# Kernel optimization log

Measured on AMD Instinct MI355X. Metric: run time of the kernel, lower is better.

Reference implementation:

```python
import jax, jax.numpy as jnp
import numpy as np

N_FEATURES = 64
D_MODEL = 256


def setup_inputs() -> dict:
    key = jax.random.key(0)
    ks = jax.random.split(key, 6)
    B = 4096
    x = jax.random.normal(ks[0], (B, N_FEATURES), dtype=jnp.float32)
    # Stacked per-feature weights (equivalent to n_features separate MLPs).
    # Linear(1, d): weight [d, 1] -> stacked as [F, d]; bias [F, d]
    s1 = 1.0  # kaiming-uniform-ish scale for fan_in=1
    W1 = jax.random.uniform(ks[1], (N_FEATURES, D_MODEL), jnp.float32, -s1, s1)
    b1 = jax.random.uniform(ks[2], (N_FEATURES, D_MODEL), jnp.float32, -s1, s1)
    # Linear(d, d): weight [d, d] per feature -> [F, d, d]
    s2 = 1.0 / np.sqrt(D_MODEL)
    W2 = jax.random.uniform(ks[3], (N_FEATURES, D_MODEL, D_MODEL), jnp.float32, -s2, s2)
    b2 = jax.random.uniform(ks[4], (N_FEATURES, D_MODEL), jnp.float32, -s2, s2)
    cls_token = jax.random.normal(ks[5], (1, 1, D_MODEL), dtype=jnp.float32)
    return {"x": x, "W1": W1, "b1": b1, "W2": W2, "b2": b2, "cls_token": cls_token}


def reference(x, W1, b1, W2, b2, cls_token):
    # h[b,f,d] = relu(x[b,f] * W1[f,d] + b1[f,d])   (Linear(1,d) per feature)
    h = jax.nn.relu(x[:, :, None] * W1[None, :, :] + b1[None, :, :])
    # out[b,f,e] = h[b,f,:] @ W2[f,:,:] + b2[f,:]   (Linear(d,d) per feature)
    out = jnp.einsum("bfd,fde->bfe", h, W2) + b2[None, :, :]
    cls = jnp.broadcast_to(cls_token, (x.shape[0], 1, out.shape[-1]))
    return jnp.concatenate([cls, out], axis=1)  # [B, F+1, d_model]
```

## Files before the change

kernel.cpp:

```cpp
#include <hip/hip_runtime.h>
#include <hip/hip_bf16.h>


#define B_  4096
#define F_  64
#define D_  256
#define ORS (65 * 256)

using f32x4  = __attribute__((ext_vector_type(4))) float;
using s16x8  = __attribute__((ext_vector_type(8))) short;

__device__ __forceinline__ unsigned short to_bf16_bits(float v) {
    __hip_bfloat16 h = __float2bfloat16(v);
    return *reinterpret_cast<unsigned short*>(&h);
}

__global__ __launch_bounds__(256) void femb_prep(
    const float* __restrict__ W2, unsigned short* __restrict__ W2r)
{
    const int blk = blockIdx.x;
    const int f   = blk >> 2;
    const int kq  = blk & 3;
    const int t   = threadIdx.x;

    const float* col = W2 + (size_t)f * D_ * D_ + (size_t)(kq * 64) * D_ + t;
    float r[64];
    #pragma unroll
    for (int j = 0; j < 64; ++j) r[j] = col[(size_t)j * D_];

    const int w   = t >> 6;
    const int nt  = (t >> 4) & 3;
    const int llo = t & 15;

    #pragma unroll
    for (int j8 = 0; j8 < 8; ++j8) {
        union { s16x8 s; unsigned short u[8]; } pk;
        #pragma unroll
        for (int e = 0; e < 8; ++e) pk.u[e] = to_bf16_bits(r[j8 * 8 + e]);
        const int ks   = kq * 2 + (j8 >> 2);
        const int lhi  = j8 & 3;
        const size_t unit = ((size_t)((f * 4 + w) * 4 + nt) * 8 + ks) * 64 + lhi * 16 + llo;
        *reinterpret_cast<s16x8*>(W2r + unit * 8) = pk.s;
    }
}

__global__ __launch_bounds__(256, 2) void femb_main10(
    const float* __restrict__ x,  const float* __restrict__ W1,
    const float* __restrict__ b1, const unsigned short* __restrict__ W2r,
    const float* __restrict__ b2, const float* __restrict__ cls,
    float* __restrict__ out)
{
    __shared__ float w1s[D_];
    __shared__ float b1s[D_];
    __shared__ float xs[512];
    __shared__ __align__(16) float eb[2][16 * 260];

    const int tid  = threadIdx.x;
    const int bid  = blockIdx.x;
    const int f    = bid & 63;
    const int row0 = (bid >> 6) << 9;

    w1s[tid] = W1[f * D_ + tid];
    b1s[tid] = b1[f * D_ + tid];
    xs[tid]       = x[(size_t)(row0 + tid) * F_ + f];
    xs[256 + tid] = x[(size_t)(row0 + 256 + tid) * F_ + f];

    const int lane = tid & 63;
    const int w    = tid >> 6;
    const int llo  = lane & 15;
    const int lhi  = lane >> 4;

    s16x8 breg[4][8];
    const unsigned short* gb = W2r + (size_t)(f * 4 + w) * 16384;
    #pragma unroll
    for (int nt = 0; nt < 4; ++nt)
        #pragma unroll
        for (int ks = 0; ks < 8; ++ks)
            breg[nt][ks] = *reinterpret_cast<const s16x8*>(
                gb + ((nt * 8 + ks) * 64 + lane) * 8);

    __syncthreads();

    f32x4 b2v  = *reinterpret_cast<const f32x4*>(&b2[f * D_ + lane * 4]);
    f32x4 clsv = *reinterpret_cast<const f32x4*>(cls + lane * 4);

#define EPI_BAR()                                                              \
    do {                                                                       \
        asm volatile("s_waitcnt lgkmcnt(0)" ::: "memory");                     \
        __builtin_amdgcn_s_barrier();                                          \
        asm volatile("" ::: "memory");                                         \
    } while (0)

    for (int ch = 0; ch < 16; ++ch) {
        const float xv0 = xs[ch * 32 + llo];
        const float xv1 = xs[ch * 32 + 16 + llo];

        f32x4 acc[2][4];
        #pragma unroll
        for (int mt = 0; mt < 2; ++mt)
            #pragma unroll
            for (int nt = 0; nt < 4; ++nt)
                acc[mt][nt] = (f32x4){0.f, 0.f, 0.f, 0.f};

        #pragma unroll
        for (int ks = 0; ks < 8; ++ks) {
            const int kg = ks * 32 + lhi * 8;
            f32x4 w1a = *reinterpret_cast<const f32x4*>(&w1s[kg]);
            f32x4 w1b = *reinterpret_cast<const f32x4*>(&w1s[kg + 4]);
            f32x4 b1a = *reinterpret_cast<const f32x4*>(&b1s[kg]);
            f32x4 b1b = *reinterpret_cast<const f32x4*>(&b1s[kg + 4]);

            s16x8 afrag[2];
            #pragma unroll
            for (int mt = 0; mt < 2; ++mt) {
                const float xv = mt ? xv1 : xv0;
                union { s16x8 sv; unsigned short u[8]; } pk;
                #pragma unroll
                for (int e = 0; e < 4; ++e) {
                    pk.u[e]     = to_bf16_bits(fmaxf(fmaf(xv, w1a[e], b1a[e]), 0.f));
                    pk.u[e + 4] = to_bf16_bits(fmaxf(fmaf(xv, w1b[e], b1b[e]), 0.f));
                }
                afrag[mt] = pk.sv;
            }

            #pragma unroll
            for (int nt = 0; nt < 4; ++nt)
                #pragma unroll
                for (int mt = 0; mt < 2; ++mt)
                    acc[mt][nt] = __builtin_amdgcn_mfma_f32_16x16x32_bf16(
                        breg[nt][ks], afrag[mt], acc[mt][nt], 0, 0, 0);
        }

        #pragma unroll
        for (int sc = 0; sc < 2; ++sc) {
            float* ebuf = eb[sc];
            #pragma unroll
            for (int nt = 0; nt < 4; ++nt)
                *reinterpret_cast<f32x4*>(
                    &ebuf[llo * 260 + w * 64 + nt * 16 + lhi * 4]) = acc[sc][nt];
            EPI_BAR();
            #pragma unroll
            for (int i = 0; i < 4; ++i) {
                const int lr = w * 4 + i;
                const size_t grow = (size_t)(row0 + ch * 32 + sc * 16 + lr);
                f32x4 v = *reinterpret_cast<const f32x4*>(&ebuf[lr * 260 + lane * 4]) + b2v;
                *reinterpret_cast<f32x4*>(out + grow * ORS + (f + 1) * D_ + lane * 4) = v;
                if (f == 0)
                    *reinterpret_cast<f32x4*>(out + grow * ORS + lane * 4) = clsv;
            }
            if (sc == 1) EPI_BAR();
        }
    }
#undef EPI_BAR
}

__global__ void femb_cls(const float* __restrict__ cls, float* __restrict__ out)
{
    int i = blockIdx.x * 256 + threadIdx.x;
    int b = i >> 6;
    int q = i & 63;
    f32x4 v = *reinterpret_cast<const f32x4*>(cls + q * 4);
    *reinterpret_cast<f32x4*>(out + (size_t)b * ORS + q * 4) = v;
}

__global__ __launch_bounds__(256, 2) void femb_main_fb(
    const float* __restrict__ x,  const float* __restrict__ W1,
    const float* __restrict__ b1, const float* __restrict__ W2,
    const float* __restrict__ b2, float* __restrict__ out)
{
    __shared__ float w1s[D_];
    __shared__ float b1s[D_];
    __shared__ float xs[128];
    __shared__ __align__(16) unsigned short bW[256][72];

    const int tid  = threadIdx.x;
    const int bid  = blockIdx.x;
    const int f    = bid & 63;
    const int row0 = (bid >> 6) << 7;

    w1s[tid] = W1[f * D_ + tid];
    b1s[tid] = b1[f * D_ + tid];
    if (tid < 128) xs[tid] = x[(size_t)(row0 + tid) * F_ + f];

    const int lane = tid & 63;
    const int wid  = tid >> 6;
    const int wm   = wid >> 1;
    const int wn   = wid & 1;
    const int llo  = lane & 15;
    const int lhi  = lane >> 4;

    __syncthreads();

    float xv[4];
    #pragma unroll
    for (int mt = 0; mt < 4; ++mt) xv[mt] = xs[wm * 64 + mt * 16 + llo];

    f32x4 acc[4][8];
    #pragma unroll
    for (int mt = 0; mt < 4; ++mt)
        #pragma unroll
        for (int nt = 0; nt < 8; ++nt)
            acc[mt][nt] = (f32x4){0.f, 0.f, 0.f, 0.f};

    const float* w2col = W2 + (size_t)f * D_ * D_ + tid;

    for (int kb = 0; kb < 4; ++kb) {
        float r[64];
        const float* p = w2col + (size_t)(kb * 64) * D_;
        #pragma unroll
        for (int j = 0; j < 64; ++j) r[j] = p[(size_t)j * D_];

        __syncthreads();
        #pragma unroll
        for (int j8 = 0; j8 < 8; ++j8) {
            union { s16x8 s; unsigned short u[8]; } pk;
            #pragma unroll
            for (int e = 0; e < 8; ++e) pk.u[e] = to_bf16_bits(r[j8 * 8 + e]);
            *reinterpret_cast<s16x8*>(&bW[tid][j8 * 8]) = pk.s;
        }
        __syncthreads();

        #pragma unroll
        for (int ks = 0; ks < 2; ++ks) {
            const int kg = kb * 64 + ks * 32 + lhi * 8;
            float w1r[8], b1r[8];
            #pragma unroll
            for (int e = 0; e < 8; ++e) { w1r[e] = w1s[kg + e]; b1r[e] = b1s[kg + e]; }

            s16x8 afrag[4];
            #pragma unroll
            for (int mt = 0; mt < 4; ++mt) {
                union { s16x8 s; unsigned short u[8]; } pk;
                #pragma unroll
                for (int e = 0; e < 8; ++e) {
                    float h = fmaf(xv[mt], w1r[e], b1r[e]);
                    pk.u[e] = to_bf16_bits(fmaxf(h, 0.f));
                }
                afrag[mt] = pk.s;
            }

            const int kl = ks * 32 + lhi * 8;
            #pragma unroll
            for (int nt = 0; nt < 8; ++nt) {
                s16x8 bfrag = *reinterpret_cast<const s16x8*>(
                    &bW[wn * 128 + nt * 16 + llo][kl]);
                #pragma unroll
                for (int mt = 0; mt < 4; ++mt)
                    acc[mt][nt] = __builtin_amdgcn_mfma_f32_16x16x32_bf16(
                        bfrag, afrag[mt], acc[mt][nt], 0, 0, 0);
            }
        }
    }

    const float* b2f = b2 + f * D_;
    float* obase = out + (size_t)(row0 + wm * 64 + llo) * ORS
                       + (f + 1) * D_ + wn * 128 + lhi * 4;
    #pragma unroll
    for (int nt = 0; nt < 8; ++nt) {
        f32x4 bv = *reinterpret_cast<const f32x4*>(&b2f[wn * 128 + nt * 16 + lhi * 4]);
        #pragma unroll
        for (int mt = 0; mt < 4; ++mt) {
            f32x4 v = acc[mt][nt] + bv;
            *reinterpret_cast<f32x4*>(obase + (size_t)mt * 16 * ORS + nt * 16) = v;
        }
    }
}

extern "C" void kernel_launch(void* const* d_in, const int* in_sizes, int n_in,
                              void* d_out, int out_size, void* d_ws, size_t ws_size,
                              hipStream_t stream)
{
    const float* x   = (const float*)d_in[0];
    const float* W1  = (const float*)d_in[1];
    const float* b1  = (const float*)d_in[2];
    const float* W2  = (const float*)d_in[3];
    const float* b2  = (const float*)d_in[4];
    const float* cls = (const float*)d_in[5];
    float* out = (float*)d_out;

    const size_t need = (size_t)F_ * D_ * D_ * sizeof(unsigned short);
    if (ws_size >= need) {
        unsigned short* W2r = (unsigned short*)d_ws;
        femb_prep<<<F_ * 4, 256, 0, stream>>>(W2, W2r);
        femb_main10<<<F_ * (B_ / 512), 256, 0, stream>>>(x, W1, b1, W2r, b2, cls, out);
    } else {
        femb_cls<<<(B_ * 64) / 256, 256, 0, stream>>>(cls, out);
        femb_main_fb<<<F_ * (B_ / 128), 256, 0, stream>>>(x, W1, b1, W2, b2, out);
    }
}
```

Baseline: 68.81 us.

## Process two features per 512-thread block for contiguous 2KB output row writes

Each block now handles two adjacent features over 256 batch rows with 8 waves, so every output row segment written is 512 contiguous floats (two features) instead of 256. The b2 bias is folded into the accumulator before the LDS staging store, and the grid doubles in rows while halving per-block chunk count. This aims to improve write coalescing and store efficiency on the output-bandwidth-bound epilogue, at the cost of larger LDS usage and an extra barrier per subchunk.

```diff
diff --git a/kernel.cpp b/kernel.cpp
--- a/kernel.cpp
+++ b/kernel.cpp
@@ -28,7 +28,7 @@
     #pragma unroll
     for (int j = 0; j < 64; ++j) r[j] = col[(size_t)j * D_];
 
-    const int w   = t >> 6;
+    const int cg  = t >> 6;
     const int nt  = (t >> 4) & 3;
     const int llo = t & 15;
 
@@ -39,39 +39,46 @@
         for (int e = 0; e < 8; ++e) pk.u[e] = to_bf16_bits(r[j8 * 8 + e]);
         const int ks   = kq * 2 + (j8 >> 2);
         const int lhi  = j8 & 3;
-        const size_t unit = ((size_t)((f * 4 + w) * 4 + nt) * 8 + ks) * 64 + lhi * 16 + llo;
+        const size_t unit = ((size_t)((f * 4 + cg) * 4 + nt) * 8 + ks) * 64 + lhi * 16 + llo;
         *reinterpret_cast<s16x8*>(W2r + unit * 8) = pk.s;
     }
 }
 
-__global__ __launch_bounds__(256, 2) void femb_main10(
+__global__ __launch_bounds__(512, 2) void femb_main11(
     const float* __restrict__ x,  const float* __restrict__ W1,
     const float* __restrict__ b1, const unsigned short* __restrict__ W2r,
     const float* __restrict__ b2, const float* __restrict__ cls,
     float* __restrict__ out)
 {
-    __shared__ float w1s[D_];
-    __shared__ float b1s[D_];
-    __shared__ float xs[512];
-    __shared__ __align__(16) float eb[2][16 * 260];
+    __shared__ float w1s[2][D_];
+    __shared__ float b1s[2][D_];
+    __shared__ float xs[2][256];
+    __shared__ __align__(16) float eb[2][16 * 516];
 
     const int tid  = threadIdx.x;
     const int bid  = blockIdx.x;
-    const int f    = bid & 63;
-    const int row0 = (bid >> 6) << 9;
-
-    w1s[tid] = W1[f * D_ + tid];
-    b1s[tid] = b1[f * D_ + tid];
-    xs[tid]       = x[(size_t)(row0 + tid) * F_ + f];
-    xs[256 + tid] = x[(size_t)(row0 + 256 + tid) * F_ + f];
+    const int fp   = bid & 31;
+    const int f0   = fp * 2;
+    const int row0 = (bid >> 5) << 8;
+
+    {
+        const int fl  = tid >> 8;
+        const int idx = tid & 255;
+        w1s[fl][idx] = W1[(f0 + fl) * D_ + idx];
+        b1s[fl][idx] = b1[(f0 + fl) * D_ + idx];
+        xs[fl][idx]  = x[(size_t)(row0 + idx) * F_ + f0 + fl];
+    }
 
     const int lane = tid & 63;
     const int w    = tid >> 6;
+    const int f2   = w >> 2;
+    const int cg   = w & 3;
     const int llo  = lane & 15;
     const int lhi  = lane >> 4;
+    const int f    = f0 + f2;
 
     s16x8 breg[4][8];
-    const unsigned short* gb = W2r + (size_t)(f * 4 + w) * 16384;
+    const unsigned short* gb = W2r + (size_t)(f * 4 + cg) * 16384;
     #pragma unroll
     for (int nt = 0; nt < 4; ++nt)
         #pragma unroll
@@ -79,10 +86,14 @@
             breg[nt][ks] = *reinterpret_cast<const s16x8*>(
                 gb + ((nt * 8 + ks) * 64 + lane) * 8);
 
+    f32x4 b2w[4];
+    #pragma unroll
+    for (int nt = 0; nt < 4; ++nt)
+        b2w[nt] = *reinterpret_cast<const f32x4*>(
+            &b2[f * D_ + cg * 64 + nt * 16 + lhi * 4]);
+    f32x4 clsv = *reinterpret_cast<const f32x4*>(cls + (tid & 63) * 4);
+
     __syncthreads();
-
-    f32x4 b2v  = *reinterpret_cast<const f32x4*>(&b2[f * D_ + lane * 4]);
-    f32x4 clsv = *reinterpret_cast<const f32x4*>(cls + lane * 4);
 
 #define EPI_BAR()                                                              \
     do {                                                                       \
@@ -91,9 +102,9 @@
         asm volatile("" ::: "memory");                                         \
     } while (0)
 
-    for (int ch = 0; ch < 16; ++ch) {
-        const float xv0 = xs[ch * 32 + llo];
-        const float xv1 = xs[ch * 32 + 16 + llo];
+    for (int ch = 0; ch < 8; ++ch) {
+        const float xv0 = xs[f2][ch * 32 + llo];
+        const float xv1 = xs[f2][ch * 32 + 16 + llo];
 
         f32x4 acc[2][4];
         #pragma unroll
@@ -105,10 +116,10 @@
         #pragma unroll
         for (int ks = 0; ks < 8; ++ks) {
             const int kg = ks * 32 + lhi * 8;
-            f32x4 w1a = *reinterpret_cast<const f32x4*>(&w1s[kg]);
-            f32x4 w1b = *reinterpret_cast<const f32x4*>(&w1s[kg + 4]);
-            f32x4 b1a = *reinterpret_cast<const f32x4*>(&b1s[kg]);
-            f32x4 b1b = *reinterpret_cast<const f32x4*>(&b1s[kg + 4]);
+            f32x4 w1a = *reinterpret_cast<const f32x4*>(&w1s[f2][kg]);
+            f32x4 w1b = *reinterpret_cast<const f32x4*>(&w1s[f2][kg + 4]);
+            f32x4 b1a = *reinterpret_cast<const f32x4*>(&b1s[f2][kg]);
+            f32x4 b1b = *reinterpret_cast<const f32x4*>(&b1s[f2][kg + 4]);
 
             s16x8 afrag[2];
             #pragma unroll
@@ -137,18 +148,21 @@
             #pragma unroll
             for (int nt = 0; nt < 4; ++nt)
                 *reinterpret_cast<f32x4*>(
-                    &ebuf[llo * 260 + w * 64 + nt * 16 + lhi * 4]) = acc[sc][nt];
+                    &ebuf[llo * 516 + f2 * 256 + cg * 64 + nt * 16 + lhi * 4])
+                    = acc[sc][nt] + b2w[nt];
             EPI_BAR();
+            const int lanepos = tid & 127;
             #pragma unroll
             for (int i = 0; i < 4; ++i) {
-                const int lr = w * 4 + i;
+                const int lr = (tid >> 7) + i * 4;
                 const size_t grow = (size_t)(row0 + ch * 32 + sc * 16 + lr);
-                f32x4 v = *reinterpret_cast<const f32x4*>(&ebuf[lr * 260 + lane * 4]) + b2v;
-                *reinterpret_cast<f32x4*>(out + grow * ORS + (f + 1) * D_ + lane * 4) = v;
-                if (f == 0)
-                    *reinterpret_cast<f32x4*>(out + grow * ORS + lane * 4) = clsv;
+                f32x4 v = *reinterpret_cast<const f32x4*>(&ebuf[lr * 516 + lanepos * 4]);
+                *reinterpret_cast<f32x4*>(
+                    out + grow * ORS + (size_t)(f0 + 1) * D_ + lanepos * 4) = v;
+                if (fp == 0 && lanepos < 64)
+                    *reinterpret_cast<f32x4*>(out + grow * ORS + lanepos * 4) = clsv;
             }
-            if (sc == 1) EPI_BAR();
+            EPI_BAR();
         }
     }
 #undef EPI_BAR
@@ -282,7 +296,7 @@
     if (ws_size >= need) {
         unsigned short* W2r = (unsigned short*)d_ws;
         femb_prep<<<F_ * 4, 256, 0, stream>>>(W2, W2r);
-        femb_main10<<<F_ * (B_ / 512), 256, 0, stream>>>(x, W1, b1, W2r, b2, cls, out);
+        femb_main11<<<32 * (B_ / 256), 512, 0, stream>>>(x, W1, b1, W2r, b2, cls, out);
     } else {
         femb_cls<<<(B_ * 64) / 256, 256, 0, stream>>>(cls, out);
         femb_main_fb<<<F_ * (B_ / 128), 256, 0, stream>>>(x, W1, b1, W2, b2, out);
```

After: 73.71 us. 1.07x slower.
